# Kernel optimization log

Hardware: AMD Instinct MI355X
Metric: run time of the kernel (lower is better)

## Reference

```python
import jax, jax.numpy as jnp
import numpy as np


def _cost_volume(image, coords, psize, ksize):
    # image: [c, h, w]; coords: [num, 2] pixel centers; returns [num, psize*psize]
    c, h, w = image.shape
    sp = psize // 2
    pad = ksize // 2 + sp
    ipad = jnp.pad(image, ((0, 0), (pad, pad), (pad, pad)))
    ky = jnp.arange(ksize)
    # top-left corner (in padded coords, before search shift) of each center patch
    rows = coords[:, 0, None, None] + ky[None, :, None]   # [num, k, 1]
    cols = coords[:, 1, None, None] + ky[None, None, :]   # [num, 1, k]
    center = ipad[:, rows + sp, cols + sp]                # [c, num, k, k]
    offs = jnp.stack(jnp.meshgrid(jnp.arange(psize), jnp.arange(psize), indexing='ij'), -1).reshape(-1, 2)

    def ssd(d):
        shifted = ipad[:, rows + d[0], cols + d[1]]       # [c, num, k, k]
        return jnp.sum((shifted - center) ** 2, axis=(0, 2, 3))  # [num]

    vol = jax.lax.map(ssd, offs)                          # [psize*psize, num]
    return vol.T


def _sim_map(image, coords, sigma, psize, ksize):
    c = image.shape[0]
    q = _cost_volume(image, coords, psize, ksize) / (c * ksize * ksize)
    q = jnp.exp(-q / jax.nn.relu(sigma) + 1e-20)          # sigma: [1] broadcasts
    return q[None]                                        # [1, num, psize*psize]


def setup_inputs() -> dict:
    key = jax.random.key(0)
    k1, k2, k3 = jax.random.split(key, 3)
    H = W = 256
    C = 3
    NUM = 2048
    return {
        "img": jax.random.normal(k1, (1, C, H, W), jnp.float32),
        "img_sr": jax.random.normal(k2, (1, C, H, W), jnp.float32),
        "sigma": jnp.array([4.0], jnp.float32),
        "coords": jax.random.randint(k3, (NUM, 2), 0, H),
        "kernel_size_search": 25,
        "kernel_size_center": 9,
    }


def reference(img, img_sr, sigma, coords, kernel_size_search, kernel_size_center):
    s = _sim_map(img[0], coords, sigma, kernel_size_search, kernel_size_center)
    s1 = _sim_map(img_sr[0], coords, sigma, kernel_size_search, kernel_size_center)
    return (s, s1)
```

## Files before the change

kernel.cpp:

```cpp
#include <hip/hip_runtime.h>
#include <hip/hip_fp16.h>

typedef unsigned int uint;
typedef __attribute__((ext_vector_type(2))) _Float16 half2_t;

#define NUM 2048
#define SP 12
#define WIN 33
#define RSTR 20
#define WA_DW (3*WIN*RSTR)
#define HS_STRIDE 14
#define HSE_DW (2*WA_DW)
#define HSO_DW (HSE_DW + WIN*HS_STRIDE)
#define PART_DW (HSO_DW + WIN*HS_STRIDE)
#define TOT_DW (PART_DW + 1050)

union U32H2 { uint u; half2_t h; };
__device__ __forceinline__ half2_t uh2(uint u){ U32H2 p; p.u=u; return p.h; }

#if __has_builtin(__builtin_amdgcn_fdot2)
__device__ __forceinline__ float fdot2(uint a, uint b, float c) {
    return __builtin_amdgcn_fdot2(uh2(a), uh2(b), c, false);
}
#else
__device__ __forceinline__ float fdot2(uint a, uint b, float c) {
    half2_t A = uh2(a), B = uh2(b);
    return fmaf((float)A.y, (float)B.y, fmaf((float)A.x, (float)B.x, c));
}
#endif

__global__ __launch_bounds__(256, 6) void simmap_kernel(
    const float* __restrict__ img, const float* __restrict__ img_sr,
    const float* __restrict__ sigma, const int* __restrict__ coords,
    float* __restrict__ out)
{
    __shared__ __align__(16) uint lds[TOT_DW];
    __half* wh = (__half*)lds;
    float*  lf = (float*)lds;

    const int n = blockIdx.x;
    const int imgid = blockIdx.y;
    const float* im = imgid ? img_sr : img;
    const int t = threadIdx.x;
    const int w = t >> 6;
    const int l = t & 63;
    const int r0 = coords[2*n];
    const int c0 = coords[2*n+1];

    if (r0 >= 16 && r0 < 240 && c0 >= 16 && c0 < 240) {
        const float* base = im + (r0-16)*256 + (c0-16);
        for (int f = t; f < WIN*WIN; f += 256) {
            int r = f / WIN, x = f - r*WIN;
            int go = r*256 + x;
            #pragma unroll
            for (int c = 0; c < 3; ++c) {
                __half hv = __float2half(base[c*65536 + go]);
                int rowh = (c*WIN + r)*40;
                wh[rowh + x] = hv;
                if (x >= 1)  wh[2*WA_DW + rowh + x - 1] = hv;
                if (x == 32) wh[rowh + 33] = __float2half(0.f);
            }
        }
    } else {
        for (int f = t; f < WIN*WIN; f += 256) {
            int r = f / WIN, x = f - r*WIN;
            int ri = r0 + r - 16, ci = c0 + x - 16;
            bool inb = (ri >= 0 && ri < 256 && ci >= 0 && ci < 256);
            int go = ri*256 + ci;
            #pragma unroll
            for (int c = 0; c < 3; ++c) {
                float v = inb ? im[c*65536 + go] : 0.f;
                __half hv = __float2half(v);
                int rowh = (c*WIN + r)*40;
                wh[rowh + x] = hv;
                if (x >= 1)  wh[2*WA_DW + rowh + x - 1] = hv;
                if (x == 32) wh[rowh + 33] = __float2half(0.f);
            }
        }
    }
    __syncthreads();

    if (w == 0 && l < WIN) {
        float sq[33];
        #pragma unroll
        for (int x = 0; x < 33; ++x) sq[x] = 0.f;
        #pragma unroll 1
        for (int c = 0; c < 3; ++c) {
            const uint* rp = lds + (uint)(c*WIN + l)*RSTR;
            uint U[17];
            { uint4 v = *(const uint4*)(rp);    U[0]=v.x;U[1]=v.y;U[2]=v.z;U[3]=v.w; }
            { uint4 v = *(const uint4*)(rp+4);  U[4]=v.x;U[5]=v.y;U[6]=v.z;U[7]=v.w; }
            { uint4 v = *(const uint4*)(rp+8);  U[8]=v.x;U[9]=v.y;U[10]=v.z;U[11]=v.w; }
            { uint4 v = *(const uint4*)(rp+12); U[12]=v.x;U[13]=v.y;U[14]=v.z;U[15]=v.w; }
            U[16] = rp[16];
            #pragma unroll
            for (int k = 0; k < 17; ++k) {
                half2_t h = uh2(U[k]);
                float x0 = (float)h.x, x1 = (float)h.y;
                sq[2*k] += x0*x0;
                if (2*k + 1 < 33) sq[2*k+1] += x1*x1;
            }
        }
        float s = 0.f;
        #pragma unroll
        for (int j = 0; j < 9; ++j) s += sq[j];
        lf[HSE_DW + l*HS_STRIDE + 0] = s;
        #pragma unroll
        for (int d = 1; d < 25; ++d) {
            s += sq[d+8] - sq[d-1];
            if (d & 1) lf[HSO_DW + l*HS_STRIDE + (d>>1)] = s;
            else       lf[HSE_DW + l*HS_STRIDE + (d>>1)] = s;
        }
    }

    const int parity = l & 1;
    const int d0e = (l < 50) ? (l >> 1) : 0;
    const uint sbase = parity ? (uint)WA_DW : 0u;

    float acc[13];
    #pragma unroll
    for (int oo = 0; oo < 13; ++oo) acc[oo] = 0.f;

    const int base  = (w == 0) ? 0 : (w == 1) ? 4 : (w == 2) ? 11 : 19;
    const int nrows = (w == 0) ? 4 : (w == 1) ? 7 : 8;

    #pragma unroll 1
    for (int ridx = base; ridx < base + nrows; ++ridx) {
        const int c = ridx / 9;
        const int i = ridx - 9*c;
        const uint* sp = lds + sbase + (uint)(c*WIN + d0e + i)*RSTR;
        uint S[17];
        { uint4 v = *(const uint4*)(sp);    S[0]=v.x;S[1]=v.y;S[2]=v.z;S[3]=v.w; }
        { uint4 v = *(const uint4*)(sp+4);  S[4]=v.x;S[5]=v.y;S[6]=v.z;S[7]=v.w; }
        { uint4 v = *(const uint4*)(sp+8);  S[8]=v.x;S[9]=v.y;S[10]=v.z;S[11]=v.w; }
        { uint4 v = *(const uint4*)(sp+12); S[12]=v.x;S[13]=v.y;S[14]=v.z;S[15]=v.w; }
        S[16] = sp[16];
        const uint* cp = lds + (uint)(c*WIN + SP + i)*RSTR;
        uint cw[5];
        { uint2 v = *(const uint2*)(cp+6); cw[0]=v.x; cw[1]=v.y; }
        { uint2 v = *(const uint2*)(cp+8); cw[2]=v.x; cw[3]=v.y; }
        cw[4] = cp[10] & 0xFFFFu;
        #pragma unroll
        for (int oo = 0; oo < 13; ++oo) {
            float a = acc[oo];
            #pragma unroll
            for (int jj = 0; jj < 5; ++jj)
                a = fdot2(S[oo + jj], cw[jj], a);
            acc[oo] = a;
        }
    }

    if (w != 0 && l < 50) {
        #pragma unroll
        for (int oo = 0; oo < 13; ++oo)
            wh[2*PART_DW + (w-1)*700 + l*14 + oo] = __float2half(acc[oo]);
    }
    __syncthreads();
    if (w != 0 || l >= 50) return;

    float cr[13];
    #pragma unroll
    for (int oo = 0; oo < 13; ++oo) {
        float s = acc[oo];
        #pragma unroll
        for (int ww = 0; ww < 3; ++ww)
            s += __half2float(wh[2*PART_DW + ww*700 + l*14 + oo]);
        cr[oo] = s;
    }

    const int d0 = l >> 1;
    const int hsb = parity ? HSO_DW : HSE_DW;
    float bs[13];
    #pragma unroll
    for (int oo = 0; oo < 13; ++oo) bs[oo] = 0.f;
    #pragma unroll
    for (int i = 0; i < 9; ++i) {
        const float* hr = lf + hsb + (d0 + i)*HS_STRIDE;
        float2 a = *(const float2*)(hr);
        float2 b = *(const float2*)(hr + 2);
        float2 c2 = *(const float2*)(hr + 4);
        float2 d2 = *(const float2*)(hr + 6);
        float2 e2 = *(const float2*)(hr + 8);
        float2 f2 = *(const float2*)(hr + 10);
        bs[0]+=a.x; bs[1]+=a.y; bs[2]+=b.x; bs[3]+=b.y;
        bs[4]+=c2.x; bs[5]+=c2.y; bs[6]+=d2.x; bs[7]+=d2.y;
        bs[8]+=e2.x; bs[9]+=e2.y; bs[10]+=f2.x; bs[11]+=f2.y;
        bs[12]+=hr[12];
    }
    float cc = 0.f;
    #pragma unroll
    for (int i = 0; i < 9; ++i) cc += lf[HSE_DW + (SP + i)*HS_STRIDE + 6];

    const float sg = fmaxf(sigma[0], 0.f);
    const float scl = -1.f / (243.f * sg);
    float* op = out + (size_t)(imgid*NUM + n)*625 + d0*25 + parity;
    #pragma unroll
    for (int oo = 0; oo < 13; ++oo) {
        if (parity && oo == 12) break;
        op[2*oo] = __expf((bs[oo] + cc - 2.f*cr[oo]) * scl + 1e-20f);
    }
}

extern "C" void kernel_launch(void* const* d_in, const int* in_sizes, int n_in,
                              void* d_out, int out_size, void* d_ws, size_t ws_size,
                              hipStream_t stream) {
    const float* img    = (const float*)d_in[0];
    const float* img_sr = (const float*)d_in[1];
    const float* sigma  = (const float*)d_in[2];
    const int*   coords = (const int*)d_in[3];
    float* out = (float*)d_out;
    dim3 grid(NUM, 2);
    simmap_kernel<<<grid, dim3(256), 0, stream>>>(img, img_sr, sigma, coords, out);
}
```

Baseline: 35.64 us.

## Reuse window LDS for partial sums and spread epilogue across all waves

Removes the dedicated partial-sum LDS region by writing packed half2 partials into the now-dead window buffer after a barrier, shrinking LDS per block and raising the launch-bounds occupancy hint from 6 to 8. The final reduction and exp epilogue is redistributed so 13 lanes in each of the four waves handle the 50 outputs instead of one wave doing all of them. This adds an extra __syncthreads and uses only 13 lanes per wave in the epilogue, and the higher occupancy target may force register spills.

```diff
diff --git a/kernel.cpp b/kernel.cpp
--- a/kernel.cpp
+++ b/kernel.cpp
@@ -12,8 +12,9 @@
 #define HS_STRIDE 14
 #define HSE_DW (2*WA_DW)
 #define HSO_DW (HSE_DW + WIN*HS_STRIDE)
-#define PART_DW (HSO_DW + WIN*HS_STRIDE)
-#define TOT_DW (PART_DW + 1050)
+#define TOT_DW (HSO_DW + WIN*HS_STRIDE)
+#define PARTS_DW WA_DW
+#define PSTR 8
 
 union U32H2 { uint u; half2_t h; };
 __device__ __forceinline__ half2_t uh2(uint u){ U32H2 p; p.u=u; return p.h; }
@@ -29,7 +30,12 @@
 }
 #endif
 
-__global__ __launch_bounds__(256, 6) void simmap_kernel(
+__device__ __forceinline__ uint packh2(float a, float b) {
+    return (uint)__half_as_ushort(__float2half(a)) |
+           ((uint)__half_as_ushort(__float2half(b)) << 16);
+}
+
+__global__ __launch_bounds__(256, 8) void simmap_kernel(
     const float* __restrict__ img, const float* __restrict__ img_sr,
     const float* __restrict__ sigma, const int* __restrict__ coords,
     float* __restrict__ out)
@@ -113,9 +119,9 @@
         }
     }
 
-    const int parity = l & 1;
+    const int lpar = l & 1;
     const int d0e = (l < 50) ? (l >> 1) : 0;
-    const uint sbase = parity ? (uint)WA_DW : 0u;
+    const uint sbase = lpar ? (uint)WA_DW : 0u;
 
     float acc[13];
     #pragma unroll
@@ -150,25 +156,43 @@
         }
     }
 
-    if (w != 0 && l < 50) {
-        #pragma unroll
-        for (int oo = 0; oo < 13; ++oo)
-            wh[2*PART_DW + (w-1)*700 + l*14 + oo] = __float2half(acc[oo]);
-    }
     __syncthreads();
-    if (w != 0 || l >= 50) return;
+
+    if (l < 50) {
+        uint* dst = lds + PARTS_DW + (uint)(w*50 + l)*PSTR;
+        uint4 p0, p1;
+        p0.x = packh2(acc[0],  acc[1]);  p0.y = packh2(acc[2],  acc[3]);
+        p0.z = packh2(acc[4],  acc[5]);  p0.w = packh2(acc[6],  acc[7]);
+        p1.x = packh2(acc[8],  acc[9]);  p1.y = packh2(acc[10], acc[11]);
+        p1.z = packh2(acc[12], 0.f);     p1.w = 0u;
+        ((uint4*)dst)[0] = p0;
+        ((uint4*)dst)[1] = p1;
+    }
+    __syncthreads();
+
+    const int T = 13*w + l;
+    if (l >= 13 || T >= 50) return;
+    const int d0 = T >> 1;
+    const int parity = T & 1;
 
     float cr[13];
     #pragma unroll
-    for (int oo = 0; oo < 13; ++oo) {
-        float s = acc[oo];
-        #pragma unroll
-        for (int ww = 0; ww < 3; ++ww)
-            s += __half2float(wh[2*PART_DW + ww*700 + l*14 + oo]);
-        cr[oo] = s;
-    }
-
-    const int d0 = l >> 1;
+    for (int oo = 0; oo < 13; ++oo) cr[oo] = 0.f;
+    #pragma unroll
+    for (int ww = 0; ww < 4; ++ww) {
+        const uint* src = lds + PARTS_DW + (uint)(ww*50 + T)*PSTR;
+        uint4 a = ((const uint4*)src)[0];
+        uint4 b = ((const uint4*)src)[1];
+        half2_t h;
+        h = uh2(a.x); cr[0] += (float)h.x; cr[1] += (float)h.y;
+        h = uh2(a.y); cr[2] += (float)h.x; cr[3] += (float)h.y;
+        h = uh2(a.z); cr[4] += (float)h.x; cr[5] += (float)h.y;
+        h = uh2(a.w); cr[6] += (float)h.x; cr[7] += (float)h.y;
+        h = uh2(b.x); cr[8] += (float)h.x; cr[9] += (float)h.y;
+        h = uh2(b.y); cr[10] += (float)h.x; cr[11] += (float)h.y;
+        h = uh2(b.z); cr[12] += (float)h.x;
+    }
+
     const int hsb = parity ? HSO_DW : HSE_DW;
     float bs[13];
     #pragma unroll
```

Measured after the change: 38.96 us. 9.3% more time.
